# Optimization experiments

Hardware: AMD Instinct MI355X
Metric: run time of the kernel (lower is better)

The kernel has to match this reference:

```python
import jax, jax.numpy as jnp
import numpy as np

H = 16            # num heads
D_NOPE = 128
D_ROPE = 64
D_V = 128
Q_LORA = 1536
KV_LORA = 512
HIDDEN = 2048
EPS = 1e-6


def rmsnorm(x, w):
    xf = x.astype(jnp.float32)
    var = jnp.mean(xf * xf, axis=-1, keepdims=True)
    return (w * (xf * jax.lax.rsqrt(var + EPS))).astype(x.dtype)


def rope_interleaved(x, cos, sin):
    # x: [B,H,S,D]; cos,sin: [S,D] -> use even-index entries as the per-pair values
    B, nH, S, D = x.shape
    cv = cos[:, 0::2].astype(jnp.float32)[None, None]  # [1,1,S,D/2]
    sv = sin[:, 0::2].astype(jnp.float32)[None, None]
    xf = x.astype(jnp.float32).reshape(B, nH, S, D // 2, 2)
    xr, xi = xf[..., 0], xf[..., 1]
    out = jnp.stack([xr * cv - xi * sv, xr * sv + xi * cv], axis=-1)
    return out.reshape(B, nH, S, D).astype(x.dtype)


def setup_inputs() -> dict:
    key = jax.random.key(0)
    ks = jax.random.split(key, 9)
    B, S = 2, 2048
    std = 0.02
    return {
        "hidden_states": jax.random.normal(ks[0], (B, S, HIDDEN), jnp.float32),
        "cos": jax.random.uniform(ks[1], (S, D_ROPE), jnp.float32),
        "sin": jax.random.uniform(ks[2], (S, D_ROPE), jnp.float32),
        "q_a_w": jax.random.normal(ks[3], (HIDDEN, Q_LORA), jnp.float32) * std,
        "q_a_ln_w": jnp.ones((Q_LORA,), jnp.float32),
        "q_b_w": jax.random.normal(ks[4], (Q_LORA, H * (D_NOPE + D_ROPE)), jnp.float32) * std,
        "kv_a_w": jax.random.normal(ks[5], (HIDDEN, KV_LORA + D_ROPE), jnp.float32) * std,
        "kv_a_ln_w": jnp.ones((KV_LORA,), jnp.float32),
        "kv_b_w": jax.random.normal(ks[6], (KV_LORA, H * (D_NOPE + D_V)), jnp.float32) * std,
        "o_w": jax.random.normal(ks[7], (H * D_V, HIDDEN), jnp.float32) * std,
    }


def reference(hidden_states, cos, sin, q_a_w, q_a_ln_w, q_b_w, kv_a_w, kv_a_ln_w, kv_b_w, o_w):
    B, S, _ = hidden_states.shape
    scale = 1.0 / np.sqrt(D_NOPE + D_ROPE)

    # Q path: low-rank down-proj, RMSNorm, up-proj
    q = rmsnorm(hidden_states @ q_a_w, q_a_ln_w) @ q_b_w
    q = q.reshape(B, S, H, D_NOPE + D_ROPE).transpose(0, 2, 1, 3)  # [B,H,S,Dq]
    q_nope, q_rope = q[..., :D_NOPE], q[..., D_NOPE:]

    # KV path: compressed kv + shared rope key
    ckv = hidden_states @ kv_a_w  # [B,S,KV_LORA+D_ROPE]
    compressed_kv, k_rope = ckv[..., :KV_LORA], ckv[..., KV_LORA:]
    k_rope = jnp.broadcast_to(k_rope[:, None], (B, H, S, D_ROPE))
    kv = rmsnorm(compressed_kv, kv_a_ln_w) @ kv_b_w
    kv = kv.reshape(B, S, H, D_NOPE + D_V).transpose(0, 2, 1, 3)  # [B,H,S,Dk+Dv]
    k_nope, value = kv[..., :D_NOPE], kv[..., D_NOPE:]

    q_rope = rope_interleaved(q_rope, cos, sin)
    k_rope = rope_interleaved(k_rope, cos, sin)

    query = jnp.concatenate([q_nope, q_rope], axis=-1)  # [B,H,S,192]
    key = jnp.concatenate([k_nope, k_rope], axis=-1)

    attn = jnp.einsum("bhqd,bhkd->bhqk", query, key) * scale
    attn = jax.nn.softmax(attn.astype(jnp.float32), axis=-1).astype(query.dtype)
    out = jnp.einsum("bhqk,bhkd->bhqd", attn, value)  # [B,H,S,Dv]
    out = out.transpose(0, 2, 1, 3).reshape(B, S, H * D_V)
    return out @ o_w
```

## Files before the change

### kernel.cpp

```cpp
#include <hip/hip_runtime.h>

typedef unsigned short u16;
typedef __bf16 bf16x8 __attribute__((ext_vector_type(8)));
typedef float f32x4 __attribute__((ext_vector_type(4)));
typedef u16 u16x4 __attribute__((ext_vector_type(4)));

#define S_ 2048

__device__ __forceinline__ u16 f2bf(float f) {
  union { float f; unsigned u; } v; v.f = f;
  unsigned r = v.u + 0x7fffu + ((v.u >> 16) & 1u);
  return (u16)(r >> 16);
}
__device__ __forceinline__ float bf2f(u16 h) {
  union { unsigned u; float f; } v; v.u = ((unsigned)h) << 16;
  return v.f;
}

__device__ __forceinline__ f32x4 mfma16(bf16x8 a, bf16x8 b, f32x4 c) {
  return __builtin_amdgcn_mfma_f32_16x16x32_bf16(a, b, c, 0, 0, 0);
}

__device__ __forceinline__ void async16(const void* g, void* l) {
  __builtin_amdgcn_global_load_lds((__attribute__((address_space(1))) void*)g,
                                   (__attribute__((address_space(3))) void*)l,
                                   16, 0, 0);
}

__global__ void cast_bf8_k(const float* __restrict__ in, u16* __restrict__ out, int n8) {
  int i = blockIdx.x * 256 + threadIdx.x;
  if (i < n8) {
    f32x4 a = ((const f32x4*)in)[2 * i], b = ((const f32x4*)in)[2 * i + 1];
    union { u16 v[8]; f32x4 q; } u;
#pragma unroll
    for (int e = 0; e < 4; ++e) { u.v[e] = f2bf(a[e]); u.v[4 + e] = f2bf(b[e]); }
    ((f32x4*)out)[i] = u.q;
  }
}

__global__ void transw_k(const float* __restrict__ W, u16* __restrict__ Wt,
                         int K, int N) {
  __shared__ float tile[32][33];
  int k0 = blockIdx.x * 32, n0 = blockIdx.y * 32;
  int tx = threadIdx.x, ty = threadIdx.y;
#pragma unroll
  for (int r = 0; r < 32; r += 8) {
    int n = n0 + tx;
    tile[ty + r][tx] = (n < N) ? W[(long)(k0 + ty + r) * N + n] : 0.f;
  }
  __syncthreads();
#pragma unroll
  for (int r = 0; r < 32; r += 8) {
    Wt[(long)(n0 + ty + r) * K + k0 + tx] = f2bf(tile[tx][ty + r]);
  }
}

__device__ __forceinline__ int xcd_chunk(int lin, int nwg) {
  if ((nwg & 7) == 0) return (lin & 7) * (nwg >> 3) + (lin >> 3);
  return lin;
}

template <typename OUT_T, bool ROPE>
__global__ __launch_bounds__(256)
void gemm_bt_k(const u16* __restrict__ A, const u16* __restrict__ Bt,
               OUT_T* __restrict__ C, int K, int Nc, int ldc,
               const float* __restrict__ cs, const float* __restrict__ sn) {
  __shared__ __align__(16) u16 sA[2][128 * 32];
  __shared__ __align__(16) u16 sB[2][128 * 32];
  int tid = threadIdx.x;
  int lane = tid & 63, w = tid >> 6;
  int wr = w >> 1, wc = w & 1;
  int l15 = lane & 15, quad = lane >> 4;
  int gx = gridDim.x;
  int nl = xcd_chunk(blockIdx.x + gx * blockIdx.y, gx * gridDim.y);
  long tm = (long)(nl / gx) * 128;
  long tn = (long)(nl % gx) * 128;
  const u16* Ab = A + tm * K;
  const u16* Bb = Bt + tn * K;
  f32x4 acc[4][4] = {};

#pragma unroll
  for (int it = 0; it < 2; ++it) {
    int c = tid + it * 256;
    int row = c >> 2, kc = c & 3;
    async16(Ab + (long)row * K + kc * 8, &sA[0][c * 8]);
    async16(Bb + (long)row * K + kc * 8, &sB[0][c * 8]);
  }

  int nk = K >> 5;
  for (int kt = 0; kt < nk; ++kt) {
    int cur = kt & 1;
    __syncthreads();
    if (kt + 1 < nk) {
      int k0n = (kt + 1) << 5;
#pragma unroll
      for (int it = 0; it < 2; ++it) {
        int c = tid + it * 256;
        int row = c >> 2, kc = c & 3;
        async16(Ab + (long)row * K + k0n + kc * 8, &sA[cur ^ 1][c * 8]);
        async16(Bb + (long)row * K + k0n + kc * 8, &sB[cur ^ 1][c * 8]);
      }
    }
    bf16x8 af[4], bfr[4];
#pragma unroll
    for (int i = 0; i < 4; ++i)
      af[i] = *(const bf16x8*)(&sA[cur][(wr * 64 + i * 16 + l15) * 32 + quad * 8]);
#pragma unroll
    for (int j = 0; j < 4; ++j)
      bfr[j] = *(const bf16x8*)(&sB[cur][(wc * 64 + j * 16 + l15) * 32 + quad * 8]);
#pragma unroll
    for (int i = 0; i < 4; ++i)
#pragma unroll
      for (int j = 0; j < 4; ++j)
        acc[i][j] = mfma16(af[i], bfr[j], acc[i][j]);
  }
#pragma unroll
  for (int i = 0; i < 4; ++i) {
#pragma unroll
    for (int j = 0; j < 4; ++j) {
      int col = (int)tn + wc * 64 + j * 16 + l15;
      if (col < Nc) {
        bool ropeT = false;
        int fi = 0;
        if constexpr (ROPE) {
          int d = col % 192;
          ropeT = (d >= 128);
          fi = (d - 128) & ~1;
        }
#pragma unroll
        for (int r = 0; r < 4; ++r) {
          long row = tm + wr * 64 + i * 16 + quad * 4 + r;
          float v = acc[i][j][r];
          if constexpr (ROPE) {
            float partner = __shfl_xor(v, 1);
            if (ropeT) {
              int si = (int)row & (S_ - 1);
              float cv = cs[si * 64 + fi], sv = sn[si * 64 + fi];
              v = (l15 & 1) ? (partner * sv + v * cv)
                            : (v * cv - partner * sv);
            }
          }
          if constexpr (sizeof(OUT_T) == 2) C[row * ldc + col] = f2bf(v);
          else                              C[row * ldc + col] = v;
        }
      }
    }
  }
}

__global__ __launch_bounds__(256)
void gemm_kvb_k(const u16* __restrict__ A, const u16* __restrict__ Bt,
                u16* __restrict__ kswz, u16* __restrict__ vswz) {
  const int K = 512;
  __shared__ __align__(16) u16 sA[2][128 * 32];
  __shared__ __align__(16) u16 sB[2][128 * 32];
  int tid = threadIdx.x;
  int lane = tid & 63, w = tid >> 6;
  int wr = w >> 1, wc = w & 1;
  int l15 = lane & 15, quad = lane >> 4;
  int gx = gridDim.x;
  int nl = xcd_chunk(blockIdx.x + gx * blockIdx.y, gx * gridDim.y);
  long tm = (long)(nl / gx) * 128;
  long tn = (long)(nl % gx) * 128;
  const u16* Ab = A + tm * K;
  const u16* Bb = Bt + tn * K;
  f32x4 acc[4][4] = {};

#pragma unroll
  for (int it = 0; it < 2; ++it) {
    int c = tid + it * 256;
    int row = c >> 2, kc = c & 3;
    async16(Ab + (long)row * K + kc * 8, &sA[0][c * 8]);
    async16(Bb + (long)row * K + kc * 8, &sB[0][c * 8]);
  }

  const int nk = K >> 5;
  for (int kt = 0; kt < nk; ++kt) {
    int cur = kt & 1;
    __syncthreads();
    if (kt + 1 < nk) {
      int k0n = (kt + 1) << 5;
#pragma unroll
      for (int it = 0; it < 2; ++it) {
        int c = tid + it * 256;
        int row = c >> 2, kc = c & 3;
        async16(Ab + (long)row * K + k0n + kc * 8, &sA[cur ^ 1][c * 8]);
        async16(Bb + (long)row * K + k0n + kc * 8, &sB[cur ^ 1][c * 8]);
      }
    }
    bf16x8 af[4], bfr[4];
#pragma unroll
    for (int i = 0; i < 4; ++i)
      af[i] = *(const bf16x8*)(&sA[cur][(wr * 64 + i * 16 + l15) * 32 + quad * 8]);
#pragma unroll
    for (int j = 0; j < 4; ++j)
      bfr[j] = *(const bf16x8*)(&sB[cur][(wc * 64 + j * 16 + l15) * 32 + quad * 8]);
#pragma unroll
    for (int i = 0; i < 4; ++i)
#pragma unroll
      for (int j = 0; j < 4; ++j)
        acc[i][j] = mfma16(af[i], bfr[j], acc[i][j]);
  }

  int h = (int)(tn >> 8);
  int b = (int)(tm >> 11);
  int tile = (b * 16 + h) * 32 + (((int)tm & 2047) >> 6) + wr;
  if ((tn & 255) == 0) {
    u16* dst = kswz + (long)tile * 12288;
#pragma unroll
    for (int i = 0; i < 4; ++i) {
#pragma unroll
      for (int j = 0; j < 4; ++j) {
        int frag = quad * 6 + wc * 2 + (j >> 1);
        int chunk = frag * 64 + ((j & 1) * 2 + (l15 >> 3)) * 16 + i * 4;
#pragma unroll
        for (int r = 0; r < 4; ++r)
          dst[(chunk + r) * 8 + (l15 & 7)] = f2bf(acc[i][j][r]);
      }
    }
  } else {
    u16* dst = vswz + (long)tile * 8192;
    int kq = quad >> 1;
    int e0 = (quad & 1) * 4;
#pragma unroll
    for (int i = 0; i < 4; ++i) {
#pragma unroll
      for (int j = 0; j < 4; ++j) {
        int frag = kq * 8 + wc * 4 + j;
        u16x4 pk;
#pragma unroll
        for (int r = 0; r < 4; ++r) pk[r] = f2bf(acc[i][j][r]);
        *(u16x4*)(dst + (frag * 64 + i * 16 + l15) * 8 + e0) = pk;
      }
    }
  }
}

__global__ __launch_bounds__(256)
void rmsnorm2_k(const float* __restrict__ qsrc, int ldq,
                const float* __restrict__ kvsrc, int ldkv,
                const float* __restrict__ wq, const float* __restrict__ wkv,
                u16* __restrict__ qout, u16* __restrict__ kvout) {
  int blk = blockIdx.x;
  const float* x; const float* wt; u16* o; int N;
  if (blk < 4096) { x = qsrc + (long)blk * ldq;  wt = wq;  o = qout + (long)blk * 1536;  N = 1536; }
  else { blk -= 4096; x = kvsrc + (long)blk * ldkv; wt = wkv; o = kvout + (long)blk * 512; N = 512; }
  float ss = 0.f;
  for (int i = threadIdx.x; i < N; i += 256) { float v = x[i]; ss += v * v; }
#pragma unroll
  for (int off = 32; off; off >>= 1) ss += __shfl_down(ss, off);
  __shared__ float red[4];
  if ((threadIdx.x & 63) == 0) red[threadIdx.x >> 6] = ss;
  __syncthreads();
  float inv = rsqrtf((red[0] + red[1] + red[2] + red[3]) / N + 1e-6f);
  for (int i = threadIdx.x; i < N; i += 256) o[i] = f2bf(wt[i] * x[i] * inv);
}

__global__ void krope_k(const float* __restrict__ src, int ld,
                        const float* __restrict__ cs, const float* __restrict__ sn,
                        u16* __restrict__ out) {
  int idx = blockIdx.x * 256 + threadIdx.x;
  int row = idx >> 5, i = idx & 31;
  int s = row & (S_ - 1);
  float xr = src[(long)row * ld + 2 * i];
  float xi = src[(long)row * ld + 2 * i + 1];
  float cv = cs[s * 64 + 2 * i], sv = sn[s * 64 + 2 * i];
  out[(long)row * 64 + 2 * i]     = f2bf(xr * cv - xi * sv);
  out[(long)row * 64 + 2 * i + 1] = f2bf(xr * sv + xi * cv);
}

__global__ void krfill_k(const u16* __restrict__ kr, u16* __restrict__ kswz) {
  int tile = blockIdx.x;
  int bh = tile >> 5, kt = tile & 31;
  int b = bh >> 4;
  u16* dst = kswz + (long)tile * 12288;
#pragma unroll
  for (int it = 0; it < 2; ++it) {
    int c = threadIdx.x + it * 256;
    int lane = c & 63, fd = c >> 6;
    int kg = fd >> 1, dbr = fd & 1;
    int sl = lane & 15;
    int key = kt * 64 + (sl >> 2) * 16 + kg * 4 + (sl & 3);
    int doff = dbr * 32 + (lane >> 4) * 8;
    int frag = kg * 6 + 4 + dbr;
    *(f32x4*)(dst + (frag * 64 + lane) * 8) =
        *(const f32x4*)(kr + ((long)(b * S_ + key)) * 64 + doff);
  }
}

__global__ __launch_bounds__(256, 2)
void attn_k(const u16* __restrict__ qb, const u16* __restrict__ kswz,
            const u16* __restrict__ vswz, u16* __restrict__ attnO) {
  int lin = blockIdx.x + 16 * blockIdx.y;
  int xcd = lin & 7;
  int j = lin >> 3;
  int bh = (xcd << 2) + (j >> 4);
  int qt = j & 15;
  int b = bh >> 4, h = bh & 15;
  int tid = threadIdx.x, lane = tid & 63, w = tid >> 6;
  int l15 = lane & 15, quad = lane >> 4;
  int qrow0 = qt * 128 + w * 32;

  __shared__ __align__(16) u16 sK[2][24 * 64 * 8];
  __shared__ __align__(16) u16 sV[2][16 * 64 * 8];

  const u16* Kb = kswz + (long)bh * 32 * 12288;
  const u16* Vb = vswz + (long)bh * 32 * 8192;

  bf16x8 qf[2][6];
#pragma unroll
  for (int rg = 0; rg < 2; ++rg) {
    const u16* qp = qb + ((long)(b * S_ + qrow0 + rg * 16 + l15)) * 3072 + h * 192 + quad * 8;
#pragma unroll
    for (int kb = 0; kb < 6; ++kb) qf[rg][kb] = *(const bf16x8*)(qp + kb * 32);
  }

  f32x4 o[2][8] = {};
  float lsum[2] = {};
  const float scale = 0.07216878364870322f;

#pragma unroll
  for (int i = 0; i < 6; ++i) { int c = tid + i * 256; async16(Kb + c * 8, &sK[0][c * 8]); }
#pragma unroll
  for (int i = 0; i < 4; ++i) { int c = tid + i * 256; async16(Vb + c * 8, &sV[0][c * 8]); }

#pragma unroll 1
  for (int kt = 0; kt < 32; ++kt) {
    int cur = kt & 1;
    __syncthreads();
    if (kt < 31) {
      const u16* Kt = Kb + (long)(kt + 1) * 12288;
      const u16* Vt = Vb + (long)(kt + 1) * 8192;
#pragma unroll
      for (int i = 0; i < 6; ++i) { int c = tid + i * 256; async16(Kt + c * 8, &sK[cur ^ 1][c * 8]); }
#pragma unroll
      for (int i = 0; i < 4; ++i) { int c = tid + i * 256; async16(Vt + c * 8, &sV[cur ^ 1][c * 8]); }
    }

    const u16* kbase = sK[cur];
    const u16* vbase = sV[cur];

    f32x4 s[2][4] = {};
#pragma unroll
    for (int kg = 0; kg < 4; ++kg) {
#pragma unroll
      for (int db = 0; db < 6; ++db) {
        bf16x8 kf = *(const bf16x8*)(kbase + ((kg * 6 + db) * 64 + lane) * 8);
        s[0][kg] = mfma16(kf, qf[0][db], s[0][kg]);
        s[1][kg] = mfma16(kf, qf[1][db], s[1][kg]);
      }
    }

    bf16x8 pf[2][2];
#pragma unroll
    for (int rg = 0; rg < 2; ++rg) {
#pragma unroll
      for (int kg = 0; kg < 4; ++kg) {
#pragma unroll
        for (int r = 0; r < 4; ++r) {
          float p = __expf(s[rg][kg][r] * scale);
          lsum[rg] += p;
          s[rg][kg][r] = p;
        }
      }
#pragma unroll
      for (int kq = 0; kq < 2; ++kq) {
        union { unsigned wd[4]; bf16x8 v; } u;
        asm("v_cvt_pk_bf16_f32 %0, %1, %2"
            : "=v"(u.wd[0]) : "v"(s[rg][2 * kq][0]), "v"(s[rg][2 * kq][1]));
        asm("v_cvt_pk_bf16_f32 %0, %1, %2"
            : "=v"(u.wd[1]) : "v"(s[rg][2 * kq][2]), "v"(s[rg][2 * kq][3]));
        asm("v_cvt_pk_bf16_f32 %0, %1, %2"
            : "=v"(u.wd[2]) : "v"(s[rg][2 * kq + 1][0]), "v"(s[rg][2 * kq + 1][1]));
        asm("v_cvt_pk_bf16_f32 %0, %1, %2"
            : "=v"(u.wd[3]) : "v"(s[rg][2 * kq + 1][2]), "v"(s[rg][2 * kq + 1][3]));
        pf[rg][kq] = u.v;
      }
    }

#pragma unroll
    for (int kq = 0; kq < 2; ++kq) {
#pragma unroll
      for (int j2 = 0; j2 < 8; ++j2) {
        bf16x8 vf = *(const bf16x8*)(vbase + ((kq * 8 + j2) * 64 + lane) * 8);
        o[0][j2] = mfma16(pf[0][kq], vf, o[0][j2]);
        o[1][j2] = mfma16(pf[1][kq], vf, o[1][j2]);
      }
    }
  }

  float invr[2][4];
#pragma unroll
  for (int rg = 0; rg < 2; ++rg) {
    float ssum = lsum[rg];
    ssum += __shfl_xor(ssum, 16);
    ssum += __shfl_xor(ssum, 32);
#pragma unroll
    for (int r = 0; r < 4; ++r)
      invr[rg][r] = 1.f / __shfl(ssum, quad * 4 + r);
  }
#pragma unroll
  for (int rg = 0; rg < 2; ++rg) {
    u16* op = attnO + ((long)(b * S_ + qrow0 + rg * 16)) * 2048 + h * 128;
#pragma unroll
    for (int j2 = 0; j2 < 8; ++j2)
#pragma unroll
      for (int r = 0; r < 4; ++r)
        op[(long)(quad * 4 + r) * 2048 + j2 * 16 + l15] = f2bf(o[rg][j2][r] * invr[rg][r]);
  }
}

extern "C" void kernel_launch(void* const* d_in, const int* in_sizes, int n_in,
                              void* d_out, int out_size, void* d_ws, size_t ws_size,
                              hipStream_t stream) {
  const float* hs      = (const float*)d_in[0];
  const float* cosb    = (const float*)d_in[1];
  const float* sinb    = (const float*)d_in[2];
  const float* q_a_w   = (const float*)d_in[3];
  const float* q_a_ln  = (const float*)d_in[4];
  const float* q_b_w   = (const float*)d_in[5];
  const float* kv_a_w  = (const float*)d_in[6];
  const float* kv_a_ln = (const float*)d_in[7];
  const float* kv_b_w  = (const float*)d_in[8];
  const float* o_w     = (const float*)d_in[9];
  float* out = (float*)d_out;
  (void)in_sizes; (void)n_in; (void)out_size; (void)ws_size;

  char* p = (char*)d_ws;
  auto alloc = [&](size_t b) { char* r = p; p += (b + 255) & ~((size_t)255); return r; };
  u16*   hs_bf  = (u16*)  alloc((size_t)4096 * 2048 * 2);
  u16*   qakvT  = (u16*)  alloc((size_t)2176 * 2048 * 2);
  u16*   qbwT   = (u16*)  alloc((size_t)3072 * 1536 * 2);
  u16*   kvbwT  = (u16*)  alloc((size_t)4096 * 512  * 2);
  u16*   owT    = (u16*)  alloc((size_t)2048 * 2048 * 2);
  float* qa_ckv = (float*)alloc((size_t)4096 * 2176 * 4);
  u16*   qan    = (u16*)  alloc((size_t)4096 * 1536 * 2);
  u16*   ckvn   = (u16*)  alloc((size_t)4096 * 512  * 2);
  u16*   kr     = (u16*)  alloc((size_t)4096 * 64   * 2);
  u16*   qbuf   = (u16*)  alloc((size_t)4096 * 3072 * 2);
  u16*   aO     = (u16*)  alloc((size_t)4096 * 2048 * 2);
  u16* kswz = (u16*)qa_ckv;
  u16* vswz = (u16*)hs_bf;

  dim3 tb(32, 8);
  cast_bf8_k<<<4096, 256, 0, stream>>>(hs, hs_bf, 4096 * 2048 / 8);
  transw_k<<<dim3(64, 48),  tb, 0, stream>>>(q_a_w,  qakvT,                     2048, 1536);
  transw_k<<<dim3(64, 20),  tb, 0, stream>>>(kv_a_w, qakvT + (long)1536 * 2048, 2048, 576);
  transw_k<<<dim3(48, 96),  tb, 0, stream>>>(q_b_w,  qbwT,  1536, 3072);
  transw_k<<<dim3(16, 128), tb, 0, stream>>>(kv_b_w, kvbwT, 512,  4096);
  transw_k<<<dim3(64, 64),  tb, 0, stream>>>(o_w,    owT,   2048, 2048);

  gemm_bt_k<float, false><<<dim3(17, 32), 256, 0, stream>>>(
      hs_bf, qakvT, qa_ckv, 2048, 2176, 2176, nullptr, nullptr);
  rmsnorm2_k<<<8192, 256, 0, stream>>>(qa_ckv, 2176, qa_ckv + 1536, 2176,
                                       q_a_ln, kv_a_ln, qan, ckvn);
  krope_k<<<512, 256, 0, stream>>>(qa_ckv + 2048, 2176, cosb, sinb, kr);
  gemm_bt_k<u16, true><<<dim3(24, 32), 256, 0, stream>>>(
      qan, qbwT, qbuf, 1536, 3072, 3072, cosb, sinb);
  gemm_kvb_k<<<dim3(32, 32), 256, 0, stream>>>(ckvn, kvbwT, kswz, vswz);
  krfill_k<<<1024, 256, 0, stream>>>(kr, kswz);
  attn_k<<<dim3(16, 32), 256, 0, stream>>>(qbuf, kswz, vswz, aO);
  gemm_bt_k<float, false><<<dim3(16, 32), 256, 0, stream>>>(
      aO, owT, out, 2048, 2048, 2048, nullptr, nullptr);
}
```

Measured before the change: 473.2 us.

## Swizzle GEMM LDS layout, prescale Q for exp2, sum softmax rows via MFMA

The GEMM kernels XOR-swizzle the 16-byte k-chunks in shared memory so the per-row fragment reads avoid bank conflicts. In the Q-projection epilogue, every column is multiplied by scale*log2(e), so attention can call exp2f directly with no per-element multiply. The softmax denominator is now accumulated with an MFMA against a vector of bf16 ones, replacing scalar adds and the cross-lane shuffles at the end. The row sums are therefore built from bf16-rounded probabilities, which slightly changes numerics. The kernel still skips max subtraction, as it did before.

Result: no change. 477.7 us (+0.9%).

```diff
diff --git a/kernel.cpp b/kernel.cpp
--- a/kernel.cpp
+++ b/kernel.cpp
@@ -26,6 +26,8 @@
                                    (__attribute__((address_space(3))) void*)l,
                                    16, 0, 0);
 }
+
+#define QSCALE2 0.10411756755f
 
 __global__ void cast_bf8_k(const float* __restrict__ in, u16* __restrict__ out, int n8) {
   int i = blockIdx.x * 256 + threadIdx.x;
@@ -82,7 +84,8 @@
 #pragma unroll
   for (int it = 0; it < 2; ++it) {
     int c = tid + it * 256;
-    int row = c >> 2, kc = c & 3;
+    int row = c >> 2, sl = c & 3;
+    int kc = sl ^ ((row >> 1) & 3);
     async16(Ab + (long)row * K + kc * 8, &sA[0][c * 8]);
     async16(Bb + (long)row * K + kc * 8, &sB[0][c * 8]);
   }
@@ -96,18 +99,25 @@
 #pragma unroll
       for (int it = 0; it < 2; ++it) {
         int c = tid + it * 256;
-        int row = c >> 2, kc = c & 3;
+        int row = c >> 2, sl = c & 3;
+        int kc = sl ^ ((row >> 1) & 3);
         async16(Ab + (long)row * K + k0n + kc * 8, &sA[cur ^ 1][c * 8]);
         async16(Bb + (long)row * K + k0n + kc * 8, &sB[cur ^ 1][c * 8]);
       }
     }
     bf16x8 af[4], bfr[4];
 #pragma unroll
-    for (int i = 0; i < 4; ++i)
-      af[i] = *(const bf16x8*)(&sA[cur][(wr * 64 + i * 16 + l15) * 32 + quad * 8]);
-#pragma unroll
-    for (int j = 0; j < 4; ++j)
-      bfr[j] = *(const bf16x8*)(&sB[cur][(wc * 64 + j * 16 + l15) * 32 + quad * 8]);
+    for (int i = 0; i < 4; ++i) {
+      int rowa = wr * 64 + i * 16 + l15;
+      int slot = quad ^ ((rowa >> 1) & 3);
+      af[i] = *(const bf16x8*)(&sA[cur][(rowa * 4 + slot) * 8]);
+    }
+#pragma unroll
+    for (int j = 0; j < 4; ++j) {
+      int rowb = wc * 64 + j * 16 + l15;
+      int slot = quad ^ ((rowb >> 1) & 3);
+      bfr[j] = *(const bf16x8*)(&sB[cur][(rowb * 4 + slot) * 8]);
+    }
 #pragma unroll
     for (int i = 0; i < 4; ++i)
 #pragma unroll
@@ -139,6 +149,7 @@
               v = (l15 & 1) ? (partner * sv + v * cv)
                             : (v * cv - partner * sv);
             }
+            v *= QSCALE2;
           }
           if constexpr (sizeof(OUT_T) == 2) C[row * ldc + col] = f2bf(v);
           else                              C[row * ldc + col] = v;
@@ -169,7 +180,8 @@
 #pragma unroll
   for (int it = 0; it < 2; ++it) {
     int c = tid + it * 256;
-    int row = c >> 2, kc = c & 3;
+    int row = c >> 2, sl = c & 3;
+    int kc = sl ^ ((row >> 1) & 3);
     async16(Ab + (long)row * K + kc * 8, &sA[0][c * 8]);
     async16(Bb + (long)row * K + kc * 8, &sB[0][c * 8]);
   }
@@ -183,18 +195,25 @@
 #pragma unroll
       for (int it = 0; it < 2; ++it) {
         int c = tid + it * 256;
-        int row = c >> 2, kc = c & 3;
+        int row = c >> 2, sl = c & 3;
+        int kc = sl ^ ((row >> 1) & 3);
         async16(Ab + (long)row * K + k0n + kc * 8, &sA[cur ^ 1][c * 8]);
         async16(Bb + (long)row * K + k0n + kc * 8, &sB[cur ^ 1][c * 8]);
       }
     }
     bf16x8 af[4], bfr[4];
 #pragma unroll
-    for (int i = 0; i < 4; ++i)
-      af[i] = *(const bf16x8*)(&sA[cur][(wr * 64 + i * 16 + l15) * 32 + quad * 8]);
-#pragma unroll
-    for (int j = 0; j < 4; ++j)
-      bfr[j] = *(const bf16x8*)(&sB[cur][(wc * 64 + j * 16 + l15) * 32 + quad * 8]);
+    for (int i = 0; i < 4; ++i) {
+      int rowa = wr * 64 + i * 16 + l15;
+      int slot = quad ^ ((rowa >> 1) & 3);
+      af[i] = *(const bf16x8*)(&sA[cur][(rowa * 4 + slot) * 8]);
+    }
+#pragma unroll
+    for (int j = 0; j < 4; ++j) {
+      int rowb = wc * 64 + j * 16 + l15;
+      int slot = quad ^ ((rowb >> 1) & 3);
+      bfr[j] = *(const bf16x8*)(&sB[cur][(rowb * 4 + slot) * 8]);
+    }
 #pragma unroll
     for (int i = 0; i < 4; ++i)
 #pragma unroll
@@ -315,9 +334,12 @@
     for (int kb = 0; kb < 6; ++kb) qf[rg][kb] = *(const bf16x8*)(qp + kb * 32);
   }
 
+  union { u16 v[8]; bf16x8 b; } ones;
+#pragma unroll
+  for (int e = 0; e < 8; ++e) ones.v[e] = 0x3F80;
+
   f32x4 o[2][8] = {};
-  float lsum[2] = {};
-  const float scale = 0.07216878364870322f;
+  f32x4 lacc[2] = {};
 
 #pragma unroll
   for (int i = 0; i < 6; ++i) { int c = tid + i * 256; async16(Kb + c * 8, &sK[0][c * 8]); }
@@ -357,11 +379,8 @@
 #pragma unroll
       for (int kg = 0; kg < 4; ++kg) {
 #pragma unroll
-        for (int r = 0; r < 4; ++r) {
-          float p = __expf(s[rg][kg][r] * scale);
-          lsum[rg] += p;
-          s[rg][kg][r] = p;
-        }
+        for (int r = 0; r < 4; ++r)
+          s[rg][kg][r] = exp2f(s[rg][kg][r]);
       }
 #pragma unroll
       for (int kq = 0; kq < 2; ++kq) {
@@ -376,6 +395,8 @@
             : "=v"(u.wd[3]) : "v"(s[rg][2 * kq + 1][2]), "v"(s[rg][2 * kq + 1][3]));
         pf[rg][kq] = u.v;
       }
+      lacc[rg] = mfma16(pf[rg][0], ones.b, lacc[rg]);
+      lacc[rg] = mfma16(pf[rg][1], ones.b, lacc[rg]);
     }
 
 #pragma unroll
@@ -389,24 +410,17 @@
     }
   }
 
-  float invr[2][4];
-#pragma unroll
-  for (int rg = 0; rg < 2; ++rg) {
-    float ssum = lsum[rg];
-    ssum += __shfl_xor(ssum, 16);
-    ssum += __shfl_xor(ssum, 32);
-#pragma unroll
-    for (int r = 0; r < 4; ++r)
-      invr[rg][r] = 1.f / __shfl(ssum, quad * 4 + r);
-  }
 #pragma unroll
   for (int rg = 0; rg < 2; ++rg) {
     u16* op = attnO + ((long)(b * S_ + qrow0 + rg * 16)) * 2048 + h * 128;
+    float invr[4];
+#pragma unroll
+    for (int r = 0; r < 4; ++r) invr[r] = 1.f / lacc[rg][r];
 #pragma unroll
     for (int j2 = 0; j2 < 8; ++j2)
 #pragma unroll
       for (int r = 0; r < 4; ++r)
-        op[(long)(quad * 4 + r) * 2048 + j2 * 16 + l15] = f2bf(o[rg][j2][r] * invr[rg][r]);
+        op[(long)(quad * 4 + r) * 2048 + j2 * 16 + l15] = f2bf(o[rg][j2][r] * invr[r]);
   }
 }
 
```
